# Performance work log

Measured on AMD Instinct MI355X. Metric: run time of the kernel, lower is better.

The kernel has to match this reference:

```python
import jax, jax.numpy as jnp
import numpy as np

B, S, C, D, SN = 32, 145, 768, 8192, 64

def setup_inputs() -> dict:
    key = jax.random.key(0)
    ks = jax.random.split(key, 12)
    h1 = jax.random.randint(ks[0], (C,), 0, D, dtype=jnp.int32)
    h2 = jax.random.randint(ks[1], (C,), 0, D, dtype=jnp.int32)
    s1 = jax.random.randint(ks[2], (C,), 0, 2, dtype=jnp.int32) * 2 - 1
    s2 = jax.random.randint(ks[3], (C,), 0, 2, dtype=jnp.int32) * 2 - 1
    return {
        'sensor': jax.random.normal(ks[4], (B, 1, SN), jnp.float32),
        'image_embeds': jax.random.normal(ks[5], (B, S, C), jnp.float32),
        'image_masks': jnp.ones((B, S), jnp.int32),
        'h1': h1, 'h2': h2, 's1': s1, 's2': s2,
        'd': D,
        'W_sensor': jax.random.normal(ks[6], (C, SN), jnp.float32) * 0.02,
        'b_sensor': jnp.zeros((C,), jnp.float32),
        'W_s2': jax.random.normal(ks[7], (S, 1), jnp.float32) * 0.02,
        'b_s2': jnp.zeros((S,), jnp.float32),
        'W_out': jax.random.normal(ks[8], (1, S), jnp.float32) * 0.02,
        'b_out': jnp.zeros((1,), jnp.float32),
        'tok_emb': jax.random.normal(ks[9], (2, C), jnp.float32) * 0.02,
    }

def _sketch(x, h, s, d):
    # count-sketch: scatter c channels into d bins with random signs
    v = x * s.astype(x.dtype)                      # [B,S,C]
    Q = jnp.zeros(x.shape[:2] + (d,), x.dtype)
    return Q.at[:, :, h].add(v)                    # duplicate hash indices accumulate

def _tsp(x, h1, h2, s1, s2, d):
    # FFT circular convolution of the two sketches
    F1 = jnp.fft.fft(_sketch(x, h1, s1, d))
    F2 = jnp.fft.fft(_sketch(x, h2, s2, d))
    return jnp.fft.ifft(F1 * F2).real              # [B,S,d]

def reference(sensor, image_embeds, image_masks, h1, h2, s1, s2, d,
              W_sensor, b_sensor, W_s2, b_s2, W_out, b_out, tok_emb):
    # sensor branch: [B,1,SN] -> [B,1,C] -> [B,C,1] -> [B,C,145] -> [B,145,C]
    se = sensor @ W_sensor.T + b_sensor
    se = jnp.swapaxes(se, 1, 2)
    se = se @ W_s2.T + b_s2
    se = jnp.swapaxes(se, 1, 2)
    # image branch: add token-type embedding (idx=1), masks define shape only
    img = image_embeds + tok_emb[1][None, None, :]
    z_x = _tsp(img, h1, h2, s1, s2, d)
    z_y = _tsp(se, h1, h2, s1, s2, d)
    ip = jnp.sum(z_x * z_y, axis=2)                # [B,S]
    bp = jnp.sign(ip) * jnp.sqrt(jnp.abs(ip) + 1e-5)
    norm = jnp.maximum(jnp.linalg.norm(bp, axis=1, keepdims=True), 1e-12)
    bp = bp / norm                                 # F.normalize p=2 dim=1
    out = bp @ W_out.T + b_out                     # [B,1]
    return out
```

## Files before the change

kernel.cpp:

```cpp
#include <hip/hip_runtime.h>
#include <hip/hip_bf16.h>
#include <math.h>

#define DD 8192
#define CC 768
#define SS 145
#define BB 32
#define SN 64
#define SROWS 160
#define NCKA 24

#define NETD 12
#define NCH 12
#define M01W 36
#define NWGD (BB*2*NETD)

#define ZT 512
#define NSL 16

typedef __attribute__((ext_vector_type(8))) short short8;
typedef __attribute__((ext_vector_type(4))) float f32x4;
typedef __attribute__((ext_vector_type(2))) float f32x2;

__device__ __forceinline__ void gload16(const void* g, void* l) {
    __builtin_amdgcn_global_load_lds(
        (const __attribute__((address_space(1))) unsigned int*)g,
        (__attribute__((address_space(3))) unsigned int*)l, 16, 0, 0);
}

__device__ __forceinline__ void kS_body(
    int b, int tid,
    const float* __restrict__ sensor, const float* __restrict__ Wsen,
    const float* __restrict__ bsen,
    const int* __restrict__ h1, const int* __restrict__ h2,
    const int* __restrict__ s1, const int* __restrict__ s2,
    float4* __restrict__ CTG, float2* __restrict__ P2G, float2* P2l,
    float* sens)
{
    if (tid < SN) sens[tid] = sensor[b*SN + tid];
    {
        float4* p4 = (float4*)P2l;
        #pragma unroll
        for (int i = 0; i < 8; ++i) p4[tid + i*512] = make_float4(0.f,0.f,0.f,0.f);
    }
    __syncthreads();

    for (int c = tid; c < CC; c += 512) {
        float u = bsen[c];
        const float4* w = (const float4*)(Wsen + (size_t)c*SN);
        #pragma unroll
        for (int n4 = 0; n4 < 16; ++n4) {
            float4 wv = w[n4];
            u += sens[4*n4+0]*wv.x + sens[4*n4+1]*wv.y
               + sens[4*n4+2]*wv.z + sens[4*n4+3]*wv.w;
        }
        float f1 = (float)s1[c], f2 = (float)s2[c];
        float4 ct;
        ct.x = u * f1; ct.y = f1; ct.z = __int_as_float(h1[c] << 3); ct.w = 0.f;
        CTG[(size_t)b*CC + c] = ct;
        int t = h2[c];
        unsafeAtomicAdd(&P2l[t].x, u * f2);
        unsafeAtomicAdd(&P2l[t].y, f2);
    }
    __syncthreads();

    {
        const float4* p4 = (const float4*)P2l;
        float4* dst = (float4*)(P2G + (size_t)b*DD);
        #pragma unroll
        for (int i = 0; i < 8; ++i) dst[tid + i*512] = p4[tid + i*512];
    }
}

__device__ __forceinline__ void kA_body(
    int bid, int tid,
    const float* __restrict__ E, const float* __restrict__ tok,
    const int* __restrict__ s1, unsigned int* __restrict__ A1u)
{
    if (tid >= 384) return;
    const int b  = bid / 10;
    const int r0 = (bid % 10) * 16;
    const int c  = 2*tid;
    const int ck = tid >> 4;
    const int c2 = tid & 15;
    const float s1a = (float)s1[c], s1b = (float)s1[c+1];
    const float ta = tok[CC + c] * s1a, tb = tok[CC + c + 1] * s1b;
    #pragma unroll
    for (int rr = 0; rr < 16; ++rr) {
        int row = r0 + rr;
        unsigned int word = 0;
        if (row < SS) {
            float2 ev = *(const float2*)&E[((size_t)b*SS + row)*CC + c];
            __hip_bfloat16 x0 = __float2bfloat16(ev.x*s1a + ta);
            __hip_bfloat16 x1 = __float2bfloat16(ev.y*s1b + tb);
            word = (unsigned int)*(unsigned short*)&x0
                 | ((unsigned int)*(unsigned short*)&x1 << 16);
        }
        int gp = (c2 >> 2) ^ (row & 3);
        A1u[((size_t)(b*NCKA + ck)*SROWS + row)*16 + gp*4 + (c2 & 3)] = word;
    }
}

__global__ __launch_bounds__(512) void kSA(
    const float* __restrict__ sensor, const float* __restrict__ Wsen,
    const float* __restrict__ bsen,
    const int* __restrict__ h1, const int* __restrict__ h2,
    const int* __restrict__ s1, const int* __restrict__ s2,
    float4* __restrict__ CTG, float2* __restrict__ P2G,
    const float* __restrict__ E, const float* __restrict__ tok,
    unsigned int* __restrict__ A1u, float* __restrict__ Q)
{
    __shared__ float2 P2l[DD];
    __shared__ float  sens[SN];
    const int bid = blockIdx.x;
    const int tid = threadIdx.x;
    if (bid < 320) {
        kA_body(bid, tid, E, tok, s1, A1u);
    } else {
        if (bid == 320) for (int i = tid; i < BB*SS; i += 512) Q[i] = 0.f;
        kS_body(bid - 320, tid, sensor, Wsen, bsen, h1, h2, s1, s2,
                CTG, P2G, P2l, sens);
    }
}

__global__ __launch_bounds__(512) void kS(
    const float* __restrict__ sensor, const float* __restrict__ Wsen,
    const float* __restrict__ bsen,
    const int* __restrict__ h1, const int* __restrict__ h2,
    const int* __restrict__ s1, const int* __restrict__ s2,
    float4* __restrict__ CTG, float2* __restrict__ P2G)
{
    __shared__ float2 P2l[DD];
    __shared__ float  sens[SN];
    kS_body(blockIdx.x, threadIdx.x, sensor, Wsen, bsen, h1, h2, s1, s2,
            CTG, P2G, P2l, sens);
}

__global__ __launch_bounds__(ZT) void kZ(
    const float4* __restrict__ CTG, const float2* __restrict__ P2G,
    unsigned int* __restrict__ ZP, unsigned short* __restrict__ Z11b)
{
    __shared__ float2 P2l[DD];

    const int bid = blockIdx.x;
    const int wg  = (bid & 7)*(BB*NSL/8) + (bid >> 3);
    const int b   = wg >> 4;
    const int dsl = wg & (NSL-1);
    const int tid = threadIdx.x;
    const bool doZ11 = (b == 0);

    {
        const float4* src = (const float4*)(P2G + (size_t)b*DD);
        float4* dst = (float4*)P2l;
        #pragma unroll
        for (int i = 0; i < 8; ++i) dst[tid + i*ZT] = src[tid + i*ZT];
    }
    __syncthreads();

    const int d  = dsl*ZT + tid;
    const int d8 = d << 3;
    const float4* ctp = CTG + (size_t)b*CC;
    f32x2 accP = {0.f, 0.f};
    float accC2 = 0.f, acc1 = 0.f;
    #pragma unroll 4
    for (int c = 0; c < CC; ++c) {
        float4 ct = ctp[c];
        int ab = (d8 - __float_as_int(ct.z)) & 65535;
        f32x2 p = *(const f32x2*)((const char*)P2l + ab);
        f32x2 uu = {ct.x, ct.x};
        accP = __builtin_elementwise_fma(uu, p, accP);
        accC2 = fmaf(ct.y, p.x, accC2);
        if (doZ11) acc1 = fmaf(ct.y, p.y, acc1);
    }
    float accU = accP.x, accC = accP.y + accC2;

    __hip_bfloat16 zu = __float2bfloat16(accU);
    __hip_bfloat16 zc = __float2bfloat16(accC);
    ZP[(size_t)b*DD + d] = (unsigned int)*(unsigned short*)&zu
                         | ((unsigned int)*(unsigned short*)&zc << 16);
    if (doZ11) {
        __hip_bfloat16 z1 = __float2bfloat16(acc1);
        Z11b[d] = *(unsigned short*)&z1;
    }
}

__global__ __launch_bounds__(512) void kM11(
    const unsigned short* __restrict__ Z11b,
    const int* __restrict__ h1, const int* __restrict__ h2,
    unsigned int* __restrict__ M11u)
{
    __shared__ unsigned short Z11l[DD];
    const int ck  = blockIdx.x;
    const int tid = threadIdx.x;
    {
        const uint4* src = (const uint4*)Z11b;
        uint4* dst = (uint4*)Z11l;
        #pragma unroll
        for (int i = 0; i < 2; ++i) dst[tid + i*512] = src[tid + i*512];
    }
    __syncthreads();

    #pragma unroll 4
    for (int i = 0; i < 24; ++i) {
        int idx = tid + i*512;
        int ep  = idx >> 4;
        int cpp = idx & 15;
        int ha = h1[ck*32 + 2*cpp];
        int hb = h1[ck*32 + 2*cpp + 1];
        int he = h2[ep];
        unsigned int lo = Z11l[(ha + he) & (DD-1)];
        unsigned int hi = Z11l[(hb + he) & (DD-1)];
        M11u[((size_t)ck*768 + ep)*16 + cpp] = lo | (hi << 16);
    }
}

__global__ __launch_bounds__(512) void kAM(
    const float* __restrict__ E, const float* __restrict__ tok,
    const int* __restrict__ s1, unsigned int* __restrict__ A1u,
    const unsigned short* __restrict__ Z11b,
    const int* __restrict__ h1, const int* __restrict__ h2,
    unsigned int* __restrict__ M11u)
{
    __shared__ unsigned short Z11l[DD];
    const int bid = blockIdx.x;
    const int tid = threadIdx.x;
    if (bid < 320) {
        kA_body(bid, tid, E, tok, s1, A1u);
    } else {
        const int ck = bid - 320;
        {
            const uint4* src = (const uint4*)Z11b;
            uint4* dst = (uint4*)Z11l;
            #pragma unroll
            for (int i = 0; i < 2; ++i) dst[tid + i*512] = src[tid + i*512];
        }
        __syncthreads();
        #pragma unroll 4
        for (int i = 0; i < 24; ++i) {
            int idx = tid + i*512;
            int ep  = idx >> 4;
            int cpp = idx & 15;
            int ha = h1[ck*32 + 2*cpp];
            int hb = h1[ck*32 + 2*cpp + 1];
            int he = h2[ep];
            unsigned int lo = Z11l[(ha + he) & (DD-1)];
            unsigned int hi = Z11l[(hb + he) & (DD-1)];
            M11u[((size_t)ck*768 + ep)*16 + cpp] = lo | (hi << 16);
        }
    }
}

__global__ __launch_bounds__(512, 4) void kD(
    const unsigned int* __restrict__ A1u,
    const unsigned short* __restrict__ M11,
    const float* __restrict__ E, const float* __restrict__ tok,
    const int* __restrict__ h1, const int* __restrict__ h2,
    const int* __restrict__ s2,
    const float* __restrict__ Ws2, const float* __restrict__ bs2,
    const unsigned int* __restrict__ ZP, float* __restrict__ Q)
{
    __shared__ __align__(16) unsigned int   ZPl[DD];
    __shared__ __align__(16) unsigned short Lt[2][SROWS*32];
    __shared__ __align__(16) unsigned int   Mt01[2][64*M01W];
    __shared__ unsigned short h1l[CC];

    const int bid = blockIdx.x;
    const int wg  = (bid & 7)*(NWGD/8) + (bid >> 3);
    const int b   = wg / 24;
    const int r   = wg % 24;
    const int ch  = r / 12;
    const int et  = r % 12;
    const int tid = threadIdx.x;
    const int e0  = et * 64;
    const int cb0 = ch * 384;

    {
        const uint4* src = (const uint4*)(ZP + (size_t)b*DD);
        uint4* dst = (uint4*)ZPl;
        #pragma unroll
        for (int i = 0; i < 4; ++i) dst[tid + i*512] = src[tid + i*512];
    }
    for (int c = tid; c < CC; c += 512) h1l[c] = (unsigned short)h1[c];

    const int lane = tid & 63;
    const int wv   = tid >> 6;
    const int esub = wv & 3;
    const int shf  = wv >> 2;
    const int l15  = lane & 15;
    const int l4   = lane >> 4;
    const int eg   = e0 + esub*16 + l15;

    int gh2[4];
    #pragma unroll
    for (int j = 0; j < 4; ++j) gh2[j] = h2[e0 + ((tid + j*512) >> 5)];
    __syncthreads();

    const char* Abase = (const char*)A1u + (size_t)b*NCKA*SROWS*64;

#define BARC() do { \
    asm volatile("s_waitcnt vmcnt(1) lgkmcnt(0)" ::: "memory"); \
    __builtin_amdgcn_sched_barrier(0); \
    __builtin_amdgcn_s_barrier(); \
    __builtin_amdgcn_sched_barrier(0); \
} while (0)

#define STAGE_A(K, BUF) { \
    const char* cbase = Abase + (size_t)(ch*NCH + (K))*SROWS*64; \
    gload16(cbase + wv*1024 + lane*16, (char*)(BUF) + wv*1024); \
    if (wv < 2) \
        gload16(cbase + 8192 + wv*1024 + lane*16, \
                (char*)(BUF) + 8192 + wv*1024); \
    }

#define GATHER(K, MT) { \
    _Pragma("unroll") \
    for (int j = 0; j < 4; ++j) { \
        int idx = tid + j*512; \
        int ge = idx >> 5, gc = idx & 31; \
        int ad = ((int)h1l[cb0 + (K)*32 + gc] + gh2[j]) & (DD-1); \
        MT[ge*M01W + gc] = ZPl[ad]; \
    } }

#define LOADB2(K) \
    (*(const short8*)&M11[((size_t)(ch*NCH + (K))*768 + eg)*32 + l4*8])

#define MFMA_STEP(LT, MT, BQ) { \
    const unsigned int* mp = &MT[(esub*16 + l15)*M01W + l4*8]; \
    uint4 p0 = *(const uint4*)mp; \
    uint4 p1 = *(const uint4*)(mp + 4); \
    union { unsigned int u[4]; short8 s; } b0, b1; \
    b0.u[0] = (p0.x & 0xffffu) | (p0.y << 16); \
    b1.u[0] = (p0.x >> 16)     | (p0.y & 0xffff0000u); \
    b0.u[1] = (p0.z & 0xffffu) | (p0.w << 16); \
    b1.u[1] = (p0.z >> 16)     | (p0.w & 0xffff0000u); \
    b0.u[2] = (p1.x & 0xffffu) | (p1.y << 16); \
    b1.u[2] = (p1.x >> 16)     | (p1.y & 0xffff0000u); \
    b0.u[3] = (p1.z & 0xffffu) | (p1.w << 16); \
    b1.u[3] = (p1.z >> 16)     | (p1.w & 0xffff0000u); \
    _Pragma("unroll") \
    for (int t = 0; t < 5; ++t) { \
        int R = shf*80 + t*16 + l15; \
        short8 af = *(const short8*)&LT[R*32 + ((l4 ^ (R & 3))*8)]; \
        acc0[t] = __builtin_amdgcn_mfma_f32_16x16x32_bf16(af, b0.s, acc0[t], 0,0,0); \
        acc1[t] = __builtin_amdgcn_mfma_f32_16x16x32_bf16(af, b1.s, acc1[t], 0,0,0); \
        acc2[t] = __builtin_amdgcn_mfma_f32_16x16x32_bf16(af, BQ,   acc2[t], 0,0,0); \
    } }

    f32x4 acc0[5], acc1[5], acc2[5];
    #pragma unroll
    for (int t = 0; t < 5; ++t) {
        acc0[t] = (f32x4){0.f,0.f,0.f,0.f};
        acc1[t] = (f32x4){0.f,0.f,0.f,0.f};
        acc2[t] = (f32x4){0.f,0.f,0.f,0.f};
    }

    short8 bqA, bqB;
    STAGE_A(0, Lt[0])
    GATHER(0, Mt01[0])
    __builtin_amdgcn_sched_barrier(0);
    bqA = LOADB2(0);
    BARC();

    #pragma unroll 1
    for (int k = 0; k < NCH; k += 2) {
        if (k + 1 < NCH) {
            STAGE_A(k + 1, Lt[1])
            GATHER(k + 1, Mt01[1])
            __builtin_amdgcn_sched_barrier(0);
            bqB = LOADB2(k + 1);
        }
        MFMA_STEP(Lt[0], Mt01[0], bqA)
        BARC();

        if (k + 2 < NCH) {
            STAGE_A(k + 2, Lt[0])
            GATHER(k + 2, Mt01[0])
            __builtin_amdgcn_sched_barrier(0);
            bqA = LOADB2(k + 2);
        }
        if (k + 1 < NCH) {
            MFMA_STEP(Lt[1], Mt01[1], bqB)
        }
        BARC();
    }
#undef BARC
#undef STAGE_A
#undef GATHER
#undef LOADB2
#undef MFMA_STEP

    const float s2e = (float)s2[eg];
    const float t2e = tok[CC + eg] * s2e;
    #pragma unroll
    for (int t = 0; t < 5; ++t) {
        #pragma unroll
        for (int rr = 0; rr < 4; ++rr) {
            int s = shf*80 + t*16 + l4*4 + rr;
            float qv = 0.f;
            if (s < SS) {
                float a2v = E[((size_t)b*SS + s)*CC + eg] * s2e + t2e;
                float w2v = Ws2[s], bbv = bs2[s];
                qv = (w2v*w2v*acc0[t][rr] + w2v*bbv*acc1[t][rr]
                      + bbv*bbv*acc2[t][rr]) * a2v;
            }
            qv += __shfl_xor(qv, 1);
            qv += __shfl_xor(qv, 2);
            qv += __shfl_xor(qv, 4);
            qv += __shfl_xor(qv, 8);
            if (l15 == 0 && s < SS)
                unsafeAtomicAdd(&Q[b*SS + s], qv);
        }
    }
}

__global__ __launch_bounds__(256) void kE(
    const float* __restrict__ Q, const float* __restrict__ Wout,
    const float* __restrict__ bout, float* __restrict__ out)
{
    __shared__ float red[8];
    const int b = blockIdx.x, tid = threadIdx.x;
    float v = 0.f, w = 0.f;
    if (tid < SS) {
        float ip = Q[b*SS + tid];
        float sg = (ip > 0.f) ? 1.f : ((ip < 0.f) ? -1.f : 0.f);
        v = sg * sqrtf(fabsf(ip) + 1e-5f);
        w = v * Wout[tid];
    }
    float sq = v * v;
    #pragma unroll
    for (int off = 32; off > 0; off >>= 1) {
        sq += __shfl_down(sq, off, 64);
        w  += __shfl_down(w,  off, 64);
    }
    if ((tid & 63) == 0) { red[tid >> 6] = sq; red[4 + (tid >> 6)] = w; }
    __syncthreads();
    if (tid == 0) {
        float ssq  = red[0] + red[1] + red[2] + red[3];
        float sw   = red[4] + red[5] + red[6] + red[7];
        float norm = fmaxf(sqrtf(ssq), 1e-12f);
        out[b] = sw / norm + bout[0];
    }
}

extern "C" void kernel_launch(void* const* d_in, const int* in_sizes, int n_in,
                              void* d_out, int out_size, void* d_ws, size_t ws_size,
                              hipStream_t stream) {
    const float* sensor = (const float*)d_in[0];
    const float* E      = (const float*)d_in[1];
    const int*   h1     = (const int*)d_in[3];
    const int*   h2     = (const int*)d_in[4];
    const int*   s1     = (const int*)d_in[5];
    const int*   s2     = (const int*)d_in[6];
    const float* Wsen   = (const float*)d_in[8];
    const float* bsen   = (const float*)d_in[9];
    const float* Ws2    = (const float*)d_in[10];
    const float* bs2    = (const float*)d_in[11];
    const float* Wout   = (const float*)d_in[12];
    const float* bout   = (const float*)d_in[13];
    const float* tok    = (const float*)d_in[14];
    float* out = (float*)d_out;

    char* ws = (char*)d_ws;
    const size_t SZ_CTG = (size_t)BB*CC*16;
    const size_t SZ_P2G = (size_t)BB*DD*8;
    const size_t SZ_ZP  = (size_t)BB*DD*4;
    const size_t SZ_Z11 = (size_t)DD*2;
    const size_t SZ_M11 = (size_t)NCKA*768*64;
    const size_t SZ_Q   = (size_t)BB*SS*4;
    const size_t SZ_A1  = (size_t)BB*NCKA*SROWS*64;
    const size_t needFused = SZ_CTG+SZ_P2G+SZ_ZP+SZ_Z11+SZ_M11+SZ_Q+SZ_A1;

    if (ws_size >= needFused) {
        float4* CTG = (float4*)ws;
        float2* P2G = (float2*)(ws + SZ_CTG);
        unsigned int*   ZP   = (unsigned int*)(ws + SZ_CTG + SZ_P2G);
        unsigned short* Z11b = (unsigned short*)((char*)ZP + SZ_ZP);
        unsigned int*   M11u = (unsigned int*)((char*)Z11b + SZ_Z11);
        float*          Q    = (float*)((char*)M11u + SZ_M11);
        unsigned int*   A1u  = (unsigned int*)((char*)Q + SZ_Q);

        kSA<<<dim3(352), dim3(512), 0, stream>>>(
            sensor, Wsen, bsen, h1, h2, s1, s2, CTG, P2G, E, tok, A1u, Q);
        kZ<<<dim3(BB*NSL), dim3(ZT), 0, stream>>>(CTG, P2G, ZP, Z11b);
        kM11<<<dim3(NCKA), dim3(512), 0, stream>>>(Z11b, h1, h2, M11u);
        kD<<<dim3(NWGD), dim3(512), 0, stream>>>(
            A1u, (const unsigned short*)M11u, E, tok, h1, h2, s2,
            Ws2, bs2, ZP, Q);
        kE<<<dim3(BB), dim3(256), 0, stream>>>(Q, Wout, bout, out);
    } else {
        float4* CTG = (float4*)ws;
        float2* P2G = (float2*)(ws + SZ_CTG);
        unsigned int* A1u = (unsigned int*)ws;
        unsigned int*   ZP   = (unsigned int*)(ws + SZ_A1);
        unsigned short* Z11b = (unsigned short*)(ws + SZ_A1 + SZ_ZP);
        unsigned int*   M11u = (unsigned int*)((char*)Z11b + SZ_Z11);
        float* Q = (float*)((char*)M11u + SZ_M11);

        hipMemsetAsync(Q, 0, SZ_Q, stream);
        kS<<<dim3(BB), dim3(512), 0, stream>>>(
            sensor, Wsen, bsen, h1, h2, s1, s2, CTG, P2G);
        kZ<<<dim3(BB*NSL), dim3(ZT), 0, stream>>>(CTG, P2G, ZP, Z11b);
        kAM<<<dim3(344), dim3(512), 0, stream>>>(
            E, tok, s1, A1u, Z11b, h1, h2, M11u);
        kD<<<dim3(NWGD), dim3(512), 0, stream>>>(
            A1u, (const unsigned short*)M11u, E, tok, h1, h2, s2,
            Ws2, bs2, ZP, Q);
        kE<<<dim3(BB), dim3(256), 0, stream>>>(Q, Wout, bout, out);
    }
}
```

Before: 158.7 us.

## Repartition kD work: drop channel split, use 48-wide e tiles with 384 threads

Restructures the kD work decomposition. Each workgroup now covers all 24 channel chunks for a 48-element e tile using 6 waves (384 threads), where before it covered half the channels for a 64-element e tile with 8 waves. The grid goes from 768 to 512 workgroups. This removes the split-channel partial sums and the duplicated ZP staging per batch, and gives each workgroup a longer K loop. The cost is fewer waves per workgroup, fewer workgroups to fill the device, and a longer serial loop per workgroup.

```diff
diff --git a/kernel.cpp b/kernel.cpp
--- a/kernel.cpp
+++ b/kernel.cpp
@@ -10,10 +10,12 @@
 #define SROWS 160
 #define NCKA 24
 
-#define NETD 12
-#define NCH 12
+#define NETD 16
+#define TND 48
+#define NCH 24
 #define M01W 36
-#define NWGD (BB*2*NETD)
+#define NTD 384
+#define NWGD (BB*NETD)
 
 #define ZT 512
 #define NSL 16
@@ -250,7 +252,7 @@
     }
 }
 
-__global__ __launch_bounds__(512, 4) void kD(
+__global__ __launch_bounds__(NTD, 4) void kD(
     const unsigned int* __restrict__ A1u,
     const unsigned short* __restrict__ M11,
     const float* __restrict__ E, const float* __restrict__ tok,
@@ -261,38 +263,34 @@
 {
     __shared__ __align__(16) unsigned int   ZPl[DD];
     __shared__ __align__(16) unsigned short Lt[2][SROWS*32];
-    __shared__ __align__(16) unsigned int   Mt01[2][64*M01W];
+    __shared__ __align__(16) unsigned int   Mt01[2][TND*M01W];
     __shared__ unsigned short h1l[CC];
 
     const int bid = blockIdx.x;
     const int wg  = (bid & 7)*(NWGD/8) + (bid >> 3);
-    const int b   = wg / 24;
-    const int r   = wg % 24;
-    const int ch  = r / 12;
-    const int et  = r % 12;
+    const int b   = wg / NETD;
+    const int et  = wg % NETD;
     const int tid = threadIdx.x;
-    const int e0  = et * 64;
-    const int cb0 = ch * 384;
+    const int e0  = et * TND;
 
     {
         const uint4* src = (const uint4*)(ZP + (size_t)b*DD);
         uint4* dst = (uint4*)ZPl;
-        #pragma unroll
-        for (int i = 0; i < 4; ++i) dst[tid + i*512] = src[tid + i*512];
-    }
-    for (int c = tid; c < CC; c += 512) h1l[c] = (unsigned short)h1[c];
+        for (int i = tid; i < DD/4; i += NTD) dst[i] = src[i];
+    }
+    for (int c = tid; c < CC; c += NTD) h1l[c] = (unsigned short)h1[c];
 
     const int lane = tid & 63;
     const int wv   = tid >> 6;
-    const int esub = wv & 3;
-    const int shf  = wv >> 2;
+    const int esub = wv % 3;
+    const int shf  = wv / 3;
     const int l15  = lane & 15;
     const int l4   = lane >> 4;
     const int eg   = e0 + esub*16 + l15;
 
     int gh2[4];
     #pragma unroll
-    for (int j = 0; j < 4; ++j) gh2[j] = h2[e0 + ((tid + j*512) >> 5)];
+    for (int j = 0; j < 4; ++j) gh2[j] = h2[e0 + ((tid + j*NTD) >> 5)];
     __syncthreads();
 
     const char* Abase = (const char*)A1u + (size_t)b*NCKA*SROWS*64;
@@ -305,24 +303,24 @@
 } while (0)
 
 #define STAGE_A(K, BUF) { \
-    const char* cbase = Abase + (size_t)(ch*NCH + (K))*SROWS*64; \
+    const char* cbase = Abase + (size_t)(K)*SROWS*64; \
     gload16(cbase + wv*1024 + lane*16, (char*)(BUF) + wv*1024); \
-    if (wv < 2) \
-        gload16(cbase + 8192 + wv*1024 + lane*16, \
-                (char*)(BUF) + 8192 + wv*1024); \
+    if (wv < 4) \
+        gload16(cbase + 6144 + wv*1024 + lane*16, \
+                (char*)(BUF) + 6144 + wv*1024); \
     }
 
 #define GATHER(K, MT) { \
     _Pragma("unroll") \
     for (int j = 0; j < 4; ++j) { \
-        int idx = tid + j*512; \
+        int idx = tid + j*NTD; \
         int ge = idx >> 5, gc = idx & 31; \
-        int ad = ((int)h1l[cb0 + (K)*32 + gc] + gh2[j]) & (DD-1); \
+        int ad = ((int)h1l[(K)*32 + gc] + gh2[j]) & (DD-1); \
         MT[ge*M01W + gc] = ZPl[ad]; \
     } }
 
 #define LOADB2(K) \
-    (*(const short8*)&M11[((size_t)(ch*NCH + (K))*768 + eg)*32 + l4*8])
+    (*(const short8*)&M11[((size_t)(K)*768 + eg)*32 + l4*8])
 
 #define MFMA_STEP(LT, MT, BQ) { \
     const unsigned int* mp = &MT[(esub*16 + l15)*M01W + l4*8]; \
@@ -483,7 +481,7 @@
             sensor, Wsen, bsen, h1, h2, s1, s2, CTG, P2G, E, tok, A1u, Q);
         kZ<<<dim3(BB*NSL), dim3(ZT), 0, stream>>>(CTG, P2G, ZP, Z11b);
         kM11<<<dim3(NCKA), dim3(512), 0, stream>>>(Z11b, h1, h2, M11u);
-        kD<<<dim3(NWGD), dim3(512), 0, stream>>>(
+        kD<<<dim3(NWGD), dim3(NTD), 0, stream>>>(
             A1u, (const unsigned short*)M11u, E, tok, h1, h2, s2,
             Ws2, bs2, ZP, Q);
         kE<<<dim3(BB), dim3(256), 0, stream>>>(Q, Wout, bout, out);
@@ -502,7 +500,7 @@
         kZ<<<dim3(BB*NSL), dim3(ZT), 0, stream>>>(CTG, P2G, ZP, Z11b);
         kAM<<<dim3(344), dim3(512), 0, stream>>>(
             E, tok, s1, A1u, Z11b, h1, h2, M11u);
-        kD<<<dim3(NWGD), dim3(512), 0, stream>>>(
+        kD<<<dim3(NWGD), dim3(NTD), 0, stream>>>(
             A1u, (const unsigned short*)M11u, E, tok, h1, h2, s2,
             Ws2, bs2, ZP, Q);
         kE<<<dim3(BB), dim3(256), 0, stream>>>(Q, Wout, bout, out);
```

New measurement: 151.6 us (median of 2 runs). 1.05x faster.
